# Kernel tuning notes

Measured on AMD Instinct MI355X. Metric: run time of the kernel, lower is better.

## Reference

```python
import jax, jax.numpy as jnp
import numpy as np

B, S, IN_DIM = 8, 4096, 1024
H, D = 16, 64          # num_heads, head_dim (attention_dim = H*D = 1024)
OUT_DIM = 1024
EPS = 1e-6
HI = jax.lax.Precision.HIGHEST


def setup_inputs() -> dict:
    key = jax.random.key(0)
    ks = jax.random.split(key, 9)
    sx = 1.0 / np.sqrt(IN_DIM)
    so = 1.0 / np.sqrt(H * D)
    return {
        "x":  jax.random.normal(ks[0], (B, S, IN_DIM), jnp.float32),
        "wq": jax.random.normal(ks[1], (IN_DIM, H, D), jnp.float32) * sx,
        "bq": jnp.zeros((H, D), jnp.float32),
        "wk": jax.random.normal(ks[2], (IN_DIM, H, D), jnp.float32) * sx,
        "bk": jnp.zeros((H, D), jnp.float32),
        "wv": jax.random.normal(ks[3], (IN_DIM, H, D), jnp.float32) * sx,
        "bv": jnp.zeros((H, D), jnp.float32),
        "wo": jax.random.normal(ks[4], (H, D, OUT_DIM), jnp.float32) * so,
        "bo": jnp.zeros((OUT_DIM,), jnp.float32),
    }


def _feature_map(t):
    return jax.nn.elu(t) + 1.0


def reference(x, wq, bq, wk, bk, wv, bv, wo, bo):
    # QKV projections: [B,S,IN] x [IN,H,D] -> [B,S,H,D]
    q = jnp.einsum('bsi,ihd->bshd', x, wq) + bq
    k = jnp.einsum('bsi,ihd->bshd', x, wk) + bk
    v = jnp.einsum('bsi,ihd->bshd', x, wv) + bv

    Q = _feature_map(q)
    K = _feature_map(k)

    # Faithful to source: KV is an elementwise K*V reduced over seq -> [B,H,D]
    KV = jnp.einsum('bshd,bshd->bhd', K, v, precision=HI)
    Ksum = jnp.sum(K, axis=1)                      # [B,H,D]
    Z = 1.0 / (Q * Ksum[:, None, :, :] + EPS)      # [B,S,H,D]
    attn = Q * KV[:, None, :, :] * Z               # [B,S,H,D]

    # output projection contracts heads and head_dim
    out = jnp.einsum('bshd,hdo->bso', attn, wo) + bo
    return jax.nn.gelu(out)  # flax default gelu is approximate=True
```

## Files before the change

kernel.cpp:

```cpp
#include <hip/hip_runtime.h>


#define SEQ   4096
#define MROWS 32768
#define KDIM  1024
#define HD    1024

typedef __bf16 bf16x8 __attribute__((ext_vector_type(8)));
typedef float floatx4 __attribute__((ext_vector_type(4)));

__device__ __forceinline__ unsigned short f2bf(float f) {
    unsigned int u = __float_as_uint(f);
    u += 0x7fffu + ((u >> 16) & 1u);
    return (unsigned short)(u >> 16);
}
__device__ __forceinline__ void cvt8(const float* __restrict__ p, unsigned short* d) {
    const float4 a = *(const float4*)p;
    const float4 b = *(const float4*)(p + 4);
    d[0] = f2bf(a.x); d[1] = f2bf(a.y); d[2] = f2bf(a.z); d[3] = f2bf(a.w);
    d[4] = f2bf(b.x); d[5] = f2bf(b.y); d[6] = f2bf(b.z); d[7] = f2bf(b.w);
}

typedef const __attribute__((address_space(1))) unsigned int* gas_t;
typedef __attribute__((address_space(3))) unsigned int* las_t;
__device__ __forceinline__ void async16(const void* g, void* l) {
    __builtin_amdgcn_global_load_lds((gas_t)g, (las_t)l, 16, 0, 0);
}

__global__ __launch_bounds__(256)
void cvt_x(const float* __restrict__ x, unsigned short* __restrict__ xb)
{
    const size_t p = ((size_t)blockIdx.x * 256 + threadIdx.x) * 8;
    union { uint4 u; unsigned short s[8]; } o;
    cvt8(x + p, o.s);
    *(uint4*)(xb + p) = o.u;
}

__global__ __launch_bounds__(256)
void transpose_w(const float* __restrict__ wk, const float* __restrict__ wv,
                 unsigned short* __restrict__ wkT, unsigned short* __restrict__ wvT)
{
    __shared__ alignas(16) unsigned short Ts[64][72];
    const float* W = blockIdx.z ? wv : wk;
    unsigned short* WT = blockIdx.z ? wvT : wkT;
    const int k0 = blockIdx.x * 64, n0 = blockIdx.y * 64;
    const int t = threadIdx.x;
    const int r4 = (t >> 4) * 4, c4 = (t & 15) * 4;
#pragma unroll
    for (int i = 0; i < 4; i++) {
        const float4 f = *(const float4*)(W + (size_t)(k0 + r4 + i) * HD + n0 + c4);
        Ts[c4 + 0][r4 + i] = f2bf(f.x);
        Ts[c4 + 1][r4 + i] = f2bf(f.y);
        Ts[c4 + 2][r4 + i] = f2bf(f.z);
        Ts[c4 + 3][r4 + i] = f2bf(f.w);
    }
    __syncthreads();
    const int rr = t >> 3, cc = (t & 7) * 8;
#pragma unroll
    for (int h = 0; h < 2; h++)
        *(uint4*)(WT + (size_t)(n0 + rr + h * 32) * KDIM + k0 + cc) =
            *(const uint4*)&Ts[rr + h * 32][cc];
}

__global__ __launch_bounds__(512, 2)
void kv_gemm_fast(const unsigned short* __restrict__ xb,
                  const unsigned short* __restrict__ wkT,
                  const unsigned short* __restrict__ wvT,
                  const float* __restrict__ bk, const float* __restrict__ bv,
                  float2* __restrict__ KVZ)
{
    __shared__ alignas(16) unsigned short As[2][256 * 64];
    __shared__ alignas(16) unsigned short Bks[2][128 * 64];
    __shared__ alignas(16) unsigned short Bvs[2][128 * 64];

    const int t = threadIdx.x;

    const int id = blockIdx.x;
    const int xcd = id & 7, o = id >> 3;
    const int mtile = xcd * 16 + (o >> 3);
    const int ntile = o & 7;
    const int m0 = mtile * 256;
    const int n0 = ntile * 128;
    const int b  = m0 >> 12;

    const int w = t >> 6, lane = t & 63;
    const int wm = w >> 1, wn = w & 1;
    const int lrow = lane & 15, quad = lane >> 4;
    const int swz = lane & 7;

    const int srow  = t >> 3;
    const int sunit = (t & 7) ^ (srow & 7);
    const unsigned short* gA = xb  + (size_t)(m0 + srow) * KDIM + sunit * 8;
    const unsigned short* gK = wkT + (size_t)(n0 + srow) * KDIM + sunit * 8;
    const unsigned short* gV = wvT + (size_t)(n0 + srow) * KDIM + sunit * 8;

#define STAGE(c, tk) do {                                                     \
        const int koff_ = (tk) * 64;                                          \
        async16(gA + koff_,                    &As[c][         t * 8]);       \
        async16(gA + koff_ +  64 * KDIM,       &As[c][ 4096 +  t * 8]);       \
        async16(gA + koff_ + 128 * KDIM,       &As[c][ 8192 +  t * 8]);       \
        async16(gA + koff_ + 192 * KDIM,       &As[c][12288 +  t * 8]);       \
        async16(gK + koff_,                    &Bks[c][        t * 8]);       \
        async16(gK + koff_ +  64 * KDIM,       &Bks[c][4096 +  t * 8]);       \
        async16(gV + koff_,                    &Bvs[c][        t * 8]);       \
        async16(gV + koff_ +  64 * KDIM,       &Bvs[c][4096 +  t * 8]);       \
    } while (0)

    STAGE(0, 0);
    STAGE(1, 1);

    floatx4 accK[4][4], accV[4][4];
#pragma unroll
    for (int i = 0; i < 4; i++)
#pragma unroll
        for (int j = 0; j < 4; j++) {
            accK[i][j] = (floatx4){0.f, 0.f, 0.f, 0.f};
            accV[i][j] = (floatx4){0.f, 0.f, 0.f, 0.f};
        }

    asm volatile("s_waitcnt vmcnt(8)" ::: "memory");
    __builtin_amdgcn_s_barrier();

    for (int tk = 0; tk < 16; ++tk) {
        const int c = tk & 1;
        const unsigned short* A  = As[c];
        const unsigned short* BK = Bks[c];
        const unsigned short* BV = Bvs[c];

#pragma unroll
        for (int kk = 0; kk < 2; ++kk) {
            bf16x8 af[4];
#pragma unroll
            for (int mi = 0; mi < 4; ++mi) {
                const int row = wm * 64 + mi * 16 + lrow;
                af[mi] = *(const bf16x8*)&A[row * 64 + (((kk * 4 + quad) ^ swz) << 3)];
            }
#pragma unroll
            for (int mat = 0; mat < 2; ++mat) {
                const unsigned short* Bp = mat ? BV : BK;
                bf16x8 bf[4];
#pragma unroll
                for (int ni = 0; ni < 4; ++ni) {
                    const int row = wn * 64 + ni * 16 + lrow;
                    bf[ni] = *(const bf16x8*)&Bp[row * 64 + (((kk * 4 + quad) ^ swz) << 3)];
                }
                __builtin_amdgcn_s_barrier();
                __builtin_amdgcn_s_setprio(1);
                if (mat == 0) {
#pragma unroll
                    for (int mi = 0; mi < 4; ++mi)
#pragma unroll
                        for (int ni = 0; ni < 4; ++ni)
                            accK[mi][ni] = __builtin_amdgcn_mfma_f32_16x16x32_bf16(
                                af[mi], bf[ni], accK[mi][ni], 0, 0, 0);
                } else {
#pragma unroll
                    for (int mi = 0; mi < 4; ++mi)
#pragma unroll
                        for (int ni = 0; ni < 4; ++ni)
                            accV[mi][ni] = __builtin_amdgcn_mfma_f32_16x16x32_bf16(
                                af[mi], bf[ni], accV[mi][ni], 0, 0, 0);
                }
                __builtin_amdgcn_s_setprio(0);
            }
        }

        __builtin_amdgcn_s_barrier();
        if (tk + 2 < 16) {
            STAGE(c, tk + 2);
            asm volatile("s_waitcnt vmcnt(8)" ::: "memory");
        } else {
            asm volatile("s_waitcnt vmcnt(0)" ::: "memory");
        }
        __builtin_amdgcn_s_barrier();
    }
#undef STAGE

#pragma unroll
    for (int ni = 0; ni < 4; ++ni) {
        const int colw = n0 + wn * 64 + ni * 16 + lrow;
        const float bkf = bk[colw];
        const float bvf = bv[colw];
        float pKV = 0.f, pK = 0.f;
#pragma unroll
        for (int mi = 0; mi < 4; ++mi) {
#pragma unroll
            for (int r = 0; r < 4; ++r) {
                const float kv = accK[mi][ni][r] + bkf;
                const float K  = (kv > 0.f) ? (kv + 1.f) : __expf(kv);
                const float vv = accV[mi][ni][r] + bvf;
                pKV += K * vv;
                pK  += K;
            }
        }
        pKV += __shfl_xor(pKV, 16, 64);
        pKV += __shfl_xor(pKV, 32, 64);
        pK  += __shfl_xor(pK, 16, 64);
        pK  += __shfl_xor(pK, 32, 64);
        if (quad == 0) {
            atomicAdd(&KVZ[b * HD + colw].x, pKV);
            atomicAdd(&KVZ[b * HD + colw].y, pK);
        }
    }
}

__global__ __launch_bounds__(256)
void kv_gemm(const float* __restrict__ x,
             const float* __restrict__ wk, const float* __restrict__ bk,
             const float* __restrict__ wv, const float* __restrict__ bv,
             float2* __restrict__ KVZ)
{
    __shared__ alignas(16) unsigned short As [128][40];
    __shared__ alignas(16) unsigned short BsK[128][40];
    __shared__ alignas(16) unsigned short BsV[128][40];

    const int t = threadIdx.x;
    const int n0 = blockIdx.x * 128;
    const int m0 = blockIdx.y * 128;
    const int b  = m0 >> 12;

    const int wave = t >> 6, lane = t & 63;
    const int wm = wave >> 1, wn = wave & 1;
    const int lrow = lane & 15, quad = lane >> 4;

    floatx4 accK[4][4], accV[4][4];
#pragma unroll
    for (int i = 0; i < 4; i++)
#pragma unroll
        for (int j = 0; j < 4; j++) {
            accK[i][j] = (floatx4){0.f, 0.f, 0.f, 0.f};
            accV[i][j] = (floatx4){0.f, 0.f, 0.f, 0.f};
        }

    const int arow0 = t >> 2, akc = (t & 3) * 8;
    const int bk0 = t >> 4, bnc = (t & 15) * 8;

    for (int k0 = 0; k0 < KDIM; k0 += 32) {
        __syncthreads();
        {
            union { uint4 u; unsigned short s[8]; } ua, ub;
            cvt8(x + (size_t)(m0 + arow0) * KDIM + k0 + akc, ua.s);
            cvt8(x + (size_t)(m0 + arow0 + 64) * KDIM + k0 + akc, ub.s);
            *(uint4*)&As[arow0][akc] = ua.u;
            *(uint4*)&As[arow0 + 64][akc] = ub.u;
        }
        {
            unsigned short k0s[8], k1s[8], v0s[8], v1s[8];
            cvt8(wk + (size_t)(k0 + bk0) * HD + n0 + bnc, k0s);
            cvt8(wk + (size_t)(k0 + bk0 + 16) * HD + n0 + bnc, k1s);
            cvt8(wv + (size_t)(k0 + bk0) * HD + n0 + bnc, v0s);
            cvt8(wv + (size_t)(k0 + bk0 + 16) * HD + n0 + bnc, v1s);
#pragma unroll
            for (int j = 0; j < 8; j++) {
                BsK[bnc + j][bk0]      = k0s[j];
                BsK[bnc + j][bk0 + 16] = k1s[j];
                BsV[bnc + j][bk0]      = v0s[j];
                BsV[bnc + j][bk0 + 16] = v1s[j];
            }
        }
        __syncthreads();

        bf16x8 af[4], bfK[4], bfV[4];
#pragma unroll
        for (int mi = 0; mi < 4; mi++)
            af[mi] = *(const bf16x8*)&As[wm * 64 + mi * 16 + lrow][quad * 8];
#pragma unroll
        for (int ni = 0; ni < 4; ni++) {
            bfK[ni] = *(const bf16x8*)&BsK[wn * 64 + ni * 16 + lrow][quad * 8];
            bfV[ni] = *(const bf16x8*)&BsV[wn * 64 + ni * 16 + lrow][quad * 8];
        }
#pragma unroll
        for (int mi = 0; mi < 4; mi++)
#pragma unroll
            for (int ni = 0; ni < 4; ni++) {
                accK[mi][ni] = __builtin_amdgcn_mfma_f32_16x16x32_bf16(
                    af[mi], bfK[ni], accK[mi][ni], 0, 0, 0);
                accV[mi][ni] = __builtin_amdgcn_mfma_f32_16x16x32_bf16(
                    af[mi], bfV[ni], accV[mi][ni], 0, 0, 0);
            }
    }

#pragma unroll
    for (int ni = 0; ni < 4; ni++) {
        const int colw = n0 + wn * 64 + ni * 16 + lrow;
        const float bkf = bk[colw];
        const float bvf = bv[colw];
        float pKV = 0.f, pK = 0.f;
#pragma unroll
        for (int mi = 0; mi < 4; mi++) {
#pragma unroll
            for (int r = 0; r < 4; r++) {
                const float kk = accK[mi][ni][r] + bkf;
                const float K  = (kk > 0.f) ? (kk + 1.f) : __expf(kk);
                const float vv = accV[mi][ni][r] + bvf;
                pKV += K * vv;
                pK  += K;
            }
        }
        pKV += __shfl_xor(pKV, 16, 64);
        pKV += __shfl_xor(pKV, 32, 64);
        pK  += __shfl_xor(pK, 16, 64);
        pK  += __shfl_xor(pK, 32, 64);
        if (quad == 0) {
            atomicAdd(&KVZ[b * HD + colw].x, pKV);
            atomicAdd(&KVZ[b * HD + colw].y, pK);
        }
    }
}

__global__ __launch_bounds__(256)
void rowgemm(const float2* __restrict__ KVZ,
             const float* __restrict__ wo, const float* __restrict__ bo,
             float* __restrict__ rowf)
{
    __shared__ float a[1024];
    __shared__ float red[4][64];
    const int t = threadIdx.x;
    const int b = blockIdx.x;
    const int o0 = blockIdx.y * 64;

    for (int c = t; c < 1024; c += 256) {
        const float2 z = KVZ[b * HD + c];
        a[c] = z.x / z.y;
    }
    __syncthreads();

    const int cs = t >> 6, oi = t & 63;
    float p = 0.f;
    const int cbeg = cs * 256;
    for (int c = cbeg; c < cbeg + 256; ++c)
        p += a[c] * wo[(size_t)c * HD + o0 + oi];
    red[cs][oi] = p;
    __syncthreads();

    if (t < 64) {
        float v = red[0][t] + red[1][t] + red[2][t] + red[3][t] + bo[o0 + t];
        const float g = 0.5f * v *
            (1.f + tanhf(0.7978845608028654f * (v + 0.044715f * v * v * v)));
        rowf[b * HD + o0 + t] = g;
    }
}

__global__ __launch_bounds__(256)
void broadcast_rows(const float* __restrict__ rowf, float* __restrict__ out)
{
    const size_t idx = (size_t)blockIdx.x * 256 + threadIdx.x;
    const size_t p = idx * 4;
    const int row = (int)(p >> 10);
    const int b = row >> 12;
    const int col = (int)(p & 1023);
    *(float4*)(out + p) = *(const float4*)(rowf + b * HD + col);
}

extern "C" void kernel_launch(void* const* d_in, const int* in_sizes, int n_in,
                              void* d_out, int out_size, void* d_ws, size_t ws_size,
                              hipStream_t stream)
{
    const float* x  = (const float*)d_in[0];
    const float* wk = (const float*)d_in[3];
    const float* bk = (const float*)d_in[4];
    const float* wv = (const float*)d_in[5];
    const float* bv = (const float*)d_in[6];
    const float* wo = (const float*)d_in[7];
    const float* bo = (const float*)d_in[8];
    float* out = (float*)d_out;

    const size_t NEED = (size_t)72 * 1024 * 1024;
    if (ws_size >= NEED) {
        unsigned short* xb  = (unsigned short*)d_ws;
        unsigned short* wkT = (unsigned short*)((char*)d_ws + (67u << 20));
        unsigned short* wvT = (unsigned short*)((char*)d_ws + (69u << 20));
        float2* KVZ = (float2*)((char*)d_ws + (71u << 20));
        float* rowf = (float*)((char*)d_ws + (71u << 20) + 65536);

        hipMemsetAsync(KVZ, 0, 8 * HD * sizeof(float2), stream);
        cvt_x<<<dim3(MROWS * KDIM / 8 / 256), 256, 0, stream>>>(x, xb);
        transpose_w<<<dim3(16, 16, 2), 256, 0, stream>>>(wk, wv, wkT, wvT);
        kv_gemm_fast<<<dim3(1024), 512, 0, stream>>>(xb, wkT, wvT, bk, bv, KVZ);
        rowgemm<<<dim3(8, 16), 256, 0, stream>>>(KVZ, wo, bo, rowf);
        broadcast_rows<<<dim3((MROWS * HD / 4) / 256), 256, 0, stream>>>(rowf, out);
    } else {
        float2* KVZ = (float2*)d_ws;
        float* rowf = (float*)((char*)d_ws + 65536);
        hipMemsetAsync(KVZ, 0, 8 * HD * sizeof(float2), stream);
        kv_gemm<<<dim3(8, 256), 256, 0, stream>>>(x, wk, bk, wv, bv, KVZ);
        rowgemm<<<dim3(8, 16), 256, 0, stream>>>(KVZ, wo, bo, rowf);
        broadcast_rows<<<dim3((MROWS * HD / 4) / 256), 256, 0, stream>>>(rowf, out);
    }
}
```

Baseline: 418.3 us.

## Switch KV GEMM to 32x32 MFMA with merged B tile; fuse rowgemm with broadcast

The K/V GEMM now uses 32x32x16 bf16 MFMA instructions with a single merged B shared tile and restructured fragment loads. This cuts the number of LDS reads and MFMA issues, and removes one barrier per phase. Separately, the row GEMM and the broadcast kernels are fused into one launch that computes the GELU row and writes it across 512 sequence rows per block. The fused kernel repeats the row GEMM 8 times per (batch, out-tile), trading that redundant compute for one fewer launch and no intermediate buffer.

```diff
diff --git a/kernel.cpp b/kernel.cpp
--- a/kernel.cpp
+++ b/kernel.cpp
@@ -5,9 +5,11 @@
 #define MROWS 32768
 #define KDIM  1024
 #define HD    1024
+#define TILES 16
 
 typedef __bf16 bf16x8 __attribute__((ext_vector_type(8)));
 typedef float floatx4 __attribute__((ext_vector_type(4)));
+typedef float floatx16 __attribute__((ext_vector_type(16)));
 
 __device__ __forceinline__ unsigned short f2bf(float f) {
     unsigned int u = __float_as_uint(f);
@@ -70,8 +72,7 @@
                   float2* __restrict__ KVZ)
 {
     __shared__ alignas(16) unsigned short As[2][256 * 64];
-    __shared__ alignas(16) unsigned short Bks[2][128 * 64];
-    __shared__ alignas(16) unsigned short Bvs[2][128 * 64];
+    __shared__ alignas(16) unsigned short Bs[2][256 * 64];
 
     const int t = threadIdx.x;
 
@@ -85,91 +86,95 @@
 
     const int w = t >> 6, lane = t & 63;
     const int wm = w >> 1, wn = w & 1;
-    const int lrow = lane & 15, quad = lane >> 4;
-    const int swz = lane & 7;
+    const int l32 = lane & 31, half = lane >> 5;
+
+    int arow[2], asw[2], brow[2], bsw[2];
+#pragma unroll
+    for (int i = 0; i < 2; i++) {
+        arow[i] = wm * 64 + i * 32 + l32;  asw[i] = arow[i] & 7;
+        brow[i] = wn * 64 + i * 32 + l32;  bsw[i] = brow[i] & 7;
+    }
 
     const int srow  = t >> 3;
     const int sunit = (t & 7) ^ (srow & 7);
-    const unsigned short* gA = xb  + (size_t)(m0 + srow) * KDIM + sunit * 8;
-    const unsigned short* gK = wkT + (size_t)(n0 + srow) * KDIM + sunit * 8;
-    const unsigned short* gV = wvT + (size_t)(n0 + srow) * KDIM + sunit * 8;
+    const unsigned short* gA[4];
+    const unsigned short* gB[4];
+#pragma unroll
+    for (int ch = 0; ch < 4; ch++)
+        gA[ch] = xb + (size_t)(m0 + ch * 64 + srow) * KDIM + sunit * 8;
+    gB[0] = wkT + (size_t)(n0 +      srow) * KDIM + sunit * 8;
+    gB[1] = wkT + (size_t)(n0 + 64 + srow) * KDIM + sunit * 8;
+    gB[2] = wvT + (size_t)(n0 +      srow) * KDIM + sunit * 8;
+    gB[3] = wvT + (size_t)(n0 + 64 + srow) * KDIM + sunit * 8;
 
 #define STAGE(c, tk) do {                                                     \
-        const int koff_ = (tk) * 64;                                          \
-        async16(gA + koff_,                    &As[c][         t * 8]);       \
-        async16(gA + koff_ +  64 * KDIM,       &As[c][ 4096 +  t * 8]);       \
-        async16(gA + koff_ + 128 * KDIM,       &As[c][ 8192 +  t * 8]);       \
-        async16(gA + koff_ + 192 * KDIM,       &As[c][12288 +  t * 8]);       \
-        async16(gK + koff_,                    &Bks[c][        t * 8]);       \
-        async16(gK + koff_ +  64 * KDIM,       &Bks[c][4096 +  t * 8]);       \
-        async16(gV + koff_,                    &Bvs[c][        t * 8]);       \
-        async16(gV + koff_ +  64 * KDIM,       &Bvs[c][4096 +  t * 8]);       \
+        const int ko_ = (tk) * 64;                                            \
+        async16(gA[0] + ko_, &As[c][         t * 8]);                         \
+        async16(gA[1] + ko_, &As[c][ 4096 +  t * 8]);                         \
+        async16(gA[2] + ko_, &As[c][ 8192 +  t * 8]);                         \
+        async16(gA[3] + ko_, &As[c][12288 +  t * 8]);                         \
+        async16(gB[0] + ko_, &Bs[c][         t * 8]);                         \
+        async16(gB[1] + ko_, &Bs[c][ 4096 +  t * 8]);                         \
+        async16(gB[2] + ko_, &Bs[c][ 8192 +  t * 8]);                         \
+        async16(gB[3] + ko_, &Bs[c][12288 +  t * 8]);                         \
     } while (0)
 
     STAGE(0, 0);
     STAGE(1, 1);
 
-    floatx4 accK[4][4], accV[4][4];
-#pragma unroll
-    for (int i = 0; i < 4; i++)
-#pragma unroll
-        for (int j = 0; j < 4; j++) {
-            accK[i][j] = (floatx4){0.f, 0.f, 0.f, 0.f};
-            accV[i][j] = (floatx4){0.f, 0.f, 0.f, 0.f};
+    floatx16 accK[2][2], accV[2][2];
+#pragma unroll
+    for (int i = 0; i < 2; i++)
+#pragma unroll
+        for (int j = 0; j < 2; j++) {
+            accK[i][j] = (floatx16)(0.f);
+            accV[i][j] = (floatx16)(0.f);
         }
 
     asm volatile("s_waitcnt vmcnt(8)" ::: "memory");
     __builtin_amdgcn_s_barrier();
 
-    for (int tk = 0; tk < 16; ++tk) {
+    for (int tk = 0; tk < TILES; ++tk) {
         const int c = tk & 1;
-        const unsigned short* A  = As[c];
-        const unsigned short* BK = Bks[c];
-        const unsigned short* BV = Bvs[c];
-
-#pragma unroll
-        for (int kk = 0; kk < 2; ++kk) {
-            bf16x8 af[4];
-#pragma unroll
-            for (int mi = 0; mi < 4; ++mi) {
-                const int row = wm * 64 + mi * 16 + lrow;
-                af[mi] = *(const bf16x8*)&A[row * 64 + (((kk * 4 + quad) ^ swz) << 3)];
+        const unsigned short* A = As[c];
+        const unsigned short* B = Bs[c];
+
+#pragma unroll
+        for (int ph = 0; ph < 2; ++ph) {
+            bf16x8 af[2][2], bK[2][2], bV[2][2];
+#pragma unroll
+            for (int k2 = 0; k2 < 2; ++k2) {
+                const int u = ((ph * 2 + k2) << 1) | half;
+#pragma unroll
+                for (int mi = 0; mi < 2; ++mi)
+                    af[mi][k2] = *(const bf16x8*)&A[arow[mi] * 64 + ((u ^ asw[mi]) << 3)];
+#pragma unroll
+                for (int ni = 0; ni < 2; ++ni) {
+                    bK[ni][k2] = *(const bf16x8*)&B[ brow[ni]        * 64 + ((u ^ bsw[ni]) << 3)];
+                    bV[ni][k2] = *(const bf16x8*)&B[(brow[ni] + 128) * 64 + ((u ^ bsw[ni]) << 3)];
+                }
             }
-#pragma unroll
-            for (int mat = 0; mat < 2; ++mat) {
-                const unsigned short* Bp = mat ? BV : BK;
-                bf16x8 bf[4];
-#pragma unroll
-                for (int ni = 0; ni < 4; ++ni) {
-                    const int row = wn * 64 + ni * 16 + lrow;
-                    bf[ni] = *(const bf16x8*)&Bp[row * 64 + (((kk * 4 + quad) ^ swz) << 3)];
-                }
-                __builtin_amdgcn_s_barrier();
-                __builtin_amdgcn_s_setprio(1);
-                if (mat == 0) {
-#pragma unroll
-                    for (int mi = 0; mi < 4; ++mi)
-#pragma unroll
-                        for (int ni = 0; ni < 4; ++ni)
-                            accK[mi][ni] = __builtin_amdgcn_mfma_f32_16x16x32_bf16(
-                                af[mi], bf[ni], accK[mi][ni], 0, 0, 0);
-                } else {
-#pragma unroll
-                    for (int mi = 0; mi < 4; ++mi)
-#pragma unroll
-                        for (int ni = 0; ni < 4; ++ni)
-                            accV[mi][ni] = __builtin_amdgcn_mfma_f32_16x16x32_bf16(
-                                af[mi], bf[ni], accV[mi][ni], 0, 0, 0);
-                }
-                __builtin_amdgcn_s_setprio(0);
-            }
+            __builtin_amdgcn_s_barrier();
+            __builtin_amdgcn_s_setprio(1);
+#pragma unroll
+            for (int k2 = 0; k2 < 2; ++k2)
+#pragma unroll
+                for (int mi = 0; mi < 2; ++mi)
+#pragma unroll
+                    for (int ni = 0; ni < 2; ++ni) {
+                        accK[mi][ni] = __builtin_amdgcn_mfma_f32_32x32x16_bf16(
+                            af[mi][k2], bK[ni][k2], accK[mi][ni], 0, 0, 0);
+                        accV[mi][ni] = __builtin_amdgcn_mfma_f32_32x32x16_bf16(
+                            af[mi][k2], bV[ni][k2], accV[mi][ni], 0, 0, 0);
+                    }
+            __builtin_amdgcn_s_setprio(0);
         }
 
         __builtin_amdgcn_s_barrier();
-        if (tk + 2 < 16) {
+        if (tk + 2 < TILES) {
             STAGE(c, tk + 2);
             asm volatile("s_waitcnt vmcnt(8)" ::: "memory");
-        } else {
+        } else if (tk == TILES - 2) {
             asm volatile("s_waitcnt vmcnt(0)" ::: "memory");
         }
         __builtin_amdgcn_s_barrier();
@@ -177,15 +182,15 @@
 #undef STAGE
 
 #pragma unroll
-    for (int ni = 0; ni < 4; ++ni) {
-        const int colw = n0 + wn * 64 + ni * 16 + lrow;
+    for (int ni = 0; ni < 2; ++ni) {
+        const int colw = n0 + wn * 64 + ni * 32 + l32;
         const float bkf = bk[colw];
         const float bvf = bv[colw];
         float pKV = 0.f, pK = 0.f;
 #pragma unroll
-        for (int mi = 0; mi < 4; ++mi) {
-#pragma unroll
-            for (int r = 0; r < 4; ++r) {
+        for (int mi = 0; mi < 2; ++mi) {
+#pragma unroll
+            for (int r = 0; r < 16; ++r) {
                 const float kv = accK[mi][ni][r] + bkf;
                 const float K  = (kv > 0.f) ? (kv + 1.f) : __expf(kv);
                 const float vv = accV[mi][ni][r] + bvf;
@@ -193,11 +198,9 @@
                 pK  += K;
             }
         }
-        pKV += __shfl_xor(pKV, 16, 64);
         pKV += __shfl_xor(pKV, 32, 64);
-        pK  += __shfl_xor(pK, 16, 64);
         pK  += __shfl_xor(pK, 32, 64);
-        if (quad == 0) {
+        if (half == 0) {
             atomicAdd(&KVZ[b * HD + colw].x, pKV);
             atomicAdd(&KVZ[b * HD + colw].y, pK);
         }
@@ -309,6 +312,45 @@
 }
 
 __global__ __launch_bounds__(256)
+void rowgemm_bcast(const float2* __restrict__ KVZ,
+                   const float* __restrict__ wo, const float* __restrict__ bo,
+                   float* __restrict__ out)
+{
+    __shared__ float a[1024];
+    __shared__ float red[4][64];
+    __shared__ float sval[64];
+    const int t = threadIdx.x;
+    const int b = blockIdx.x;
+    const int o0 = blockIdx.y * 64;
+    const int s0 = blockIdx.z * 512;
+
+    for (int c = t; c < 1024; c += 256) {
+        const float2 z = KVZ[b * HD + c];
+        a[c] = z.x / z.y;
+    }
+    __syncthreads();
+
+    const int cs = t >> 6, oi = t & 63;
+    float p = 0.f;
+    const int cbeg = cs * 256;
+    for (int c = cbeg; c < cbeg + 256; ++c)
+        p += a[c] * wo[(size_t)c * HD + o0 + oi];
+    red[cs][oi] = p;
+    __syncthreads();
+
+    if (t < 64) {
+        float v = red[0][t] + red[1][t] + red[2][t] + red[3][t] + bo[o0 + t];
+        sval[t] = 0.5f * v *
+            (1.f + tanhf(0.7978845608028654f * (v + 0.044715f * v * v * v)));
+    }
+    __syncthreads();
+
+    const float4 sv4 = *(const float4*)&sval[(t & 15) * 4];
+    for (int r = t >> 4; r < 512; r += 16)
+        *(float4*)&out[((size_t)(b * SEQ + s0 + r)) * HD + o0 + (t & 15) * 4] = sv4;
+}
+
+__global__ __launch_bounds__(256)
 void rowgemm(const float2* __restrict__ KVZ,
              const float* __restrict__ wo, const float* __restrict__ bo,
              float* __restrict__ rowf)
@@ -371,14 +413,12 @@
         unsigned short* wkT = (unsigned short*)((char*)d_ws + (67u << 20));
         unsigned short* wvT = (unsigned short*)((char*)d_ws + (69u << 20));
         float2* KVZ = (float2*)((char*)d_ws + (71u << 20));
-        float* rowf = (float*)((char*)d_ws + (71u << 20) + 65536);
 
         hipMemsetAsync(KVZ, 0, 8 * HD * sizeof(float2), stream);
         cvt_x<<<dim3(MROWS * KDIM / 8 / 256), 256, 0, stream>>>(x, xb);
         transpose_w<<<dim3(16, 16, 2), 256, 0, stream>>>(wk, wv, wkT, wvT);
         kv_gemm_fast<<<dim3(1024), 512, 0, stream>>>(xb, wkT, wvT, bk, bv, KVZ);
-        rowgemm<<<dim3(8, 16), 256, 0, stream>>>(KVZ, wo, bo, rowf);
-        broadcast_rows<<<dim3((MROWS * HD / 4) / 256), 256, 0, stream>>>(rowf, out);
+        rowgemm_bcast<<<dim3(8, 16, 8), 256, 0, stream>>>(KVZ, wo, bo, out);
     } else {
         float2* KVZ = (float2*)d_ws;
         float* rowf = (float*)((char*)d_ws + 65536);
```

Result: no change. 422.7 us (+1.1%).
